# Optimization experiments

Hardware: AMD Instinct MI355X
Metric: run time of the kernel (lower is better)

Reference implementation:

```python
import jax, jax.numpy as jnp
import numpy as np
from jax import lax

EPS = 1e-06
K = 7  # kernel_size
C1 = 0.01 ** 2
C2 = 0.03 ** 2

_SOBEL_X = jnp.array([[-1.0, 0.0, 1.0], [-2.0, 0.0, 2.0], [-1.0, 0.0, 1.0]], dtype=jnp.float32).reshape(1, 1, 3, 3)
_SOBEL_Y = jnp.array([[-1.0, -2.0, -1.0], [0.0, 0.0, 0.0], [1.0, 2.0, 1.0]], dtype=jnp.float32).reshape(1, 1, 3, 3)


def _conv3x3(x, w):
    # NCHW cross-correlation with zero padding=1 (matches F.conv2d)
    return lax.conv_general_dilated(
        x, w, window_strides=(1, 1), padding=[(1, 1), (1, 1)],
        dimension_numbers=('NCHW', 'OIHW', 'NCHW'))


def _box(x):
    # avg_pool2d(k, stride=1, pad=k//2, count_include_pad=True):
    # sum over zero-padded window, divide by k*k everywhere.
    p = K // 2
    s = lax.reduce_window(x, jnp.float32(0.0), lax.add,
                          window_dimensions=(1, 1, K, K),
                          window_strides=(1, 1, 1, 1),
                          padding=[(0, 0), (0, 0), (p, p), (p, p)])
    return s / jnp.float32(K * K)


def _grad_mag(x):
    gx = _conv3x3(x, _SOBEL_X)
    gy = _conv3x3(x, _SOBEL_Y)
    return jnp.sqrt(gx * gx + gy * gy + EPS)


def setup_inputs() -> dict:
    key = jax.random.key(0)
    k1, k2 = jax.random.split(key)
    B, H, W = 64, 512, 512
    pred = jax.random.normal(k1, (B, 1, H, W), dtype=jnp.float32)
    target = jax.random.normal(k2, (B, 1, H, W), dtype=jnp.float32)
    min_target = jnp.zeros((B,), dtype=jnp.float32)
    max_target = jnp.ones((B,), dtype=jnp.float32)
    return {"pred": pred, "target": target, "min_target": min_target, "max_target": max_target}


def reference(pred, target, min_target, max_target):
    B = pred.shape[0]
    mn = min_target.reshape(B, 1, 1, 1)
    mx = max_target.reshape(B, 1, 1, 1)
    dr = jnp.maximum(mx - mn, EPS)
    p = (pred - mn) / dr
    t = (target - mn) / dr

    gp = _grad_mag(p)
    gt = _grad_mag(t)

    mu_p = _box(p)
    mu_t = _box(t)
    luminance = (2.0 * mu_p * mu_t + C1) / (mu_p * mu_p + mu_t * mu_t + C1)

    mu_gp = _box(gp)
    mu_gt = _box(gt)
    sig_p = _box(gp * gp) - mu_gp * mu_gp
    sig_t = _box(gt * gt) - mu_gt * mu_gt
    sig_x = _box(gp * gt) - mu_gp * mu_gt
    cs = (2.0 * sig_x + C2) / (sig_p + sig_t + C2)

    return 1.0 - jnp.mean(luminance * cs)
```

## Files before the change

### kernel.cpp

```cpp
#include <hip/hip_runtime.h>
#include <hip/hip_fp16.h>
#include <math.h>


constexpr int NT = 256;
constexpr float EPS_F = 1e-6f;
constexpr float C1S = 2401.0f * 0.0001f;
constexpr float C2S = 2401.0f * 0.0009f;

union U4 { uint4 u; __half2 h[4]; };
union F4U { float4 v; float a[4]; };

__device__ __forceinline__ __half2 h2swap(__half2 x) {
    unsigned u = __builtin_bit_cast(unsigned, x);
    u = (u >> 16) | (u << 16);
    return __builtin_bit_cast(__half2, u);
}

__device__ __forceinline__ float ssim_px(__half2 apt, __half2 ag, __half2 agg, __half2 agx) {
    float2 vpt = __half22float2(apt);
    float2 vg  = __half22float2(ag);
    float2 vgg = __half22float2(agg);
    float  vgx = __low2float(agx);
    float lum_n = 2.0f * vpt.x * vpt.y + C1S;
    float lum_d = vpt.x * vpt.x + vpt.y * vpt.y + C1S;
    float cs_n  = 2.0f * (49.0f * vgx - vg.x * vg.y) + C2S;
    float cs_d  = 49.0f * (vgg.x + vgg.y) - vg.x * vg.x - vg.y * vg.y + C2S;
    return lum_n * cs_n * __builtin_amdgcn_rcpf(lum_d * cs_d);
}

__global__ __launch_bounds__(NT, 4)
void gssim_strip(const float* __restrict__ pred, const float* __restrict__ target,
                 const float* __restrict__ mn_arr, const float* __restrict__ mx_arr,
                 float* __restrict__ partial) {
    constexpr int H = 512, W = 512;
    __shared__ alignas(16) __half2 spt[40][44];
    __shared__ alignas(16) __half2 sg[38][40];
    __shared__ alignas(16) __half2 hsAll[38][32][4];

    const int blk  = blockIdx.x;
    const int b    = blk >> 5;
    const int rem  = blk & 31;
    const int gy0  = (rem >> 1) * 32;
    const int tx0  = (rem & 1) * 8;
    const int tid  = threadIdx.x;

    const float mn     = mn_arr[b];
    const float inv_dr = 1.0f / fmaxf(mx_arr[b] - mn, EPS_F);
    const __half2 mn2  = __float2half2_rn(mn);
    const __half2 inv2 = __float2half2_rn(inv_dr);
    const float* pimg = pred   + (size_t)b * H * W;
    const float* timg = target + (size_t)b * H * W;

    const bool rows_ok_all = (gy0 >= 4) && (gy0 + 35 < H);

    const int gS  = tid % 10;
    const int yr  = tid / 10;
    const int yS0 = 2 * yr, yS1 = yS0 + 1;
    const int gyS0 = gy0 - 4 + yS0;
    const int gyS1 = gyS0 + 1;
    const bool rok0 = (gyS0 >= 0 && gyS0 < H);
    const bool rok1 = (gyS1 >= 0 && gyS1 < H);
    const bool hasS = (tid < 200);

    F4U Pa0, Ta0, Pa1, Ta1;

    auto stage1m = [&](int gx0n, bool rowok, int gyI, F4U& P, F4U& T) {
        int gx = gx0n - 4 + 4 * gS;
        P.v = make_float4(0.f, 0.f, 0.f, 0.f);
        T.v = make_float4(0.f, 0.f, 0.f, 0.f);
        if (rowok) {
            if (gx >= 0 && gx + 4 <= W) {
                P.v = *reinterpret_cast<const float4*>(pimg + (size_t)gyI * W + gx);
                T.v = *reinterpret_cast<const float4*>(timg + (size_t)gyI * W + gx);
            } else {
#pragma unroll
                for (int c = 0; c < 4; ++c) {
                    int x = gx + c;
                    if (x >= 0 && x < W) {
                        P.a[c] = pimg[(size_t)gyI * W + x];
                        T.a[c] = timg[(size_t)gyI * W + x];
                    }
                }
            }
        }
    };
    auto stagePair = [&](int gx0n) {
        if (rows_ok_all && gx0n >= 4 && gx0n <= 448) {
            int gx = gx0n - 4 + 4 * gS;
            Pa0.v = *reinterpret_cast<const float4*>(pimg + (size_t)gyS0 * W + gx);
            Ta0.v = *reinterpret_cast<const float4*>(timg + (size_t)gyS0 * W + gx);
            Pa1.v = *reinterpret_cast<const float4*>(pimg + (size_t)gyS1 * W + gx);
            Ta1.v = *reinterpret_cast<const float4*>(timg + (size_t)gyS1 * W + gx);
        } else {
            stage1m(gx0n, rok0, gyS0, Pa0, Ta0);
            stage1m(gx0n, rok1, gyS1, Pa1, Ta1);
        }
    };

    auto normh2 = [&](float p, float t) {
        return __hmul2(__hsub2(__floats2half2_rn(p, t), mn2), inv2);
    };
    auto writePair = [&](int gx0n) {
        U4 w0, w1;
        if (rows_ok_all && gx0n >= 4 && gx0n <= 448) {
#pragma unroll
            for (int c = 0; c < 4; ++c) {
                w0.h[c] = normh2(Pa0.a[c], Ta0.a[c]);
                w1.h[c] = normh2(Pa1.a[c], Ta1.a[c]);
            }
        } else {
            int gx = gx0n - 4 + 4 * gS;
            const __half2 zero2l = __float2half2_rn(0.0f);
#pragma unroll
            for (int c = 0; c < 4; ++c) {
                int x = gx + c;
                bool okc = (x >= 0) && (x < W);
                w0.h[c] = (rok0 && okc) ? normh2(Pa0.a[c], Ta0.a[c]) : zero2l;
                w1.h[c] = (rok1 && okc) ? normh2(Pa1.a[c], Ta1.a[c]) : zero2l;
            }
        }
        *reinterpret_cast<uint4*>(&spt[yS0][4 * gS]) = w0.u;
        *reinterpret_cast<uint4*>(&spt[yS1][4 * gS]) = w1.u;
    };

    const __half2 two2  = __float2half2_rn(2.0f);
    const __half2 eps2  = __float2half2_rn(1e-6f);
    const __half2 zero2 = __float2half2_rn(0.0f);

    if (hasS) { stagePair(tx0 * 32); writePair(tx0 * 32); }
    __syncthreads();

    float accl = 0.0f;

    for (int tt = 0; tt < 8; ++tt) {
        const int gx0 = (tx0 + tt) * 32;
        const bool interior = rows_ok_all && (gx0 >= 32) && (gx0 <= 448);

        if (tt < 7 && hasS) stagePair(gx0 + 32);

        if (tid < 190) {
            const int g  = tid % 10, kr = tid / 10;
            const int j0 = 4 * g, k0 = 2 * kr;
            __half2 a[4][6];
#pragma unroll
            for (int r = 0; r < 4; ++r) {
                U4 v; v.u = *reinterpret_cast<const uint4*>(&spt[k0 + r][j0]);
                a[r][0] = v.h[0]; a[r][1] = v.h[1]; a[r][2] = v.h[2]; a[r][3] = v.h[3];
                uint2 v2 = *reinterpret_cast<const uint2*>(&spt[k0 + r][j0 + 4]);
                a[r][4] = __builtin_bit_cast(__half2, v2.x);
                a[r][5] = __builtin_bit_cast(__half2, v2.y);
            }
            if (interior) {
#pragma unroll
                for (int rr = 0; rr < 2; ++rr) {
                    const int k = k0 + rr;
                    U4 w;
#pragma unroll
                    for (int c = 0; c < 4; ++c) {
                        __half2 gxh = __hsub2(a[rr][c + 2], a[rr][c]);
                        gxh = __hfma2(two2, __hsub2(a[rr + 1][c + 2], a[rr + 1][c]), gxh);
                        gxh = __hadd2(gxh, __hsub2(a[rr + 2][c + 2], a[rr + 2][c]));
                        __half2 gyh = __hsub2(a[rr + 2][c], a[rr][c]);
                        gyh = __hfma2(two2, __hsub2(a[rr + 2][c + 1], a[rr][c + 1]), gyh);
                        gyh = __hadd2(gyh, __hsub2(a[rr + 2][c + 2], a[rr][c + 2]));
                        w.h[c] = h2sqrt(__hfma2(gxh, gxh, __hfma2(gyh, gyh, eps2)));
                    }
                    *reinterpret_cast<uint4*>(&sg[k][j0]) = w.u;
                }
            } else {
                bool cm[4];
#pragma unroll
                for (int c = 0; c < 4; ++c) {
                    int gc = gx0 + j0 + c - 3;
                    cm[c] = (gc >= 0 && gc < W);
                }
#pragma unroll
                for (int rr = 0; rr < 2; ++rr) {
                    const int k = k0 + rr;
                    const int gr = gy0 + k - 3;
                    U4 w; w.h[0] = zero2; w.h[1] = zero2; w.h[2] = zero2; w.h[3] = zero2;
                    if (gr >= 0 && gr < H) {
#pragma unroll
                        for (int c = 0; c < 4; ++c) {
                            __half2 gxh = __hsub2(a[rr][c + 2], a[rr][c]);
                            gxh = __hfma2(two2, __hsub2(a[rr + 1][c + 2], a[rr + 1][c]), gxh);
                            gxh = __hadd2(gxh, __hsub2(a[rr + 2][c + 2], a[rr + 2][c]));
                            __half2 gyh = __hsub2(a[rr + 2][c], a[rr][c]);
                            gyh = __hfma2(two2, __hsub2(a[rr + 2][c + 1], a[rr][c + 1]), gyh);
                            gyh = __hadd2(gyh, __hsub2(a[rr + 2][c + 2], a[rr][c + 2]));
                            __half2 mag = h2sqrt(__hfma2(gxh, gxh, __hfma2(gyh, gyh, eps2)));
                            w.h[c] = cm[c] ? mag : zero2;
                        }
                    }
                    *reinterpret_cast<uint4*>(&sg[k][j0]) = w.u;
                }
            }
        }
        __syncthreads();

        auto p3unit = [&](int t) {
            const int cg = t / 38;
            const int k  = t - cg * 38;
            const int c0 = 4 * cg;
            __half2 ptv[12], sgv[12];
#pragma unroll
            for (int q = 0; q < 3; ++q) {
                U4 v; v.u = *reinterpret_cast<const uint4*>(&spt[k + 1][c0 + 4 * q]);
                ptv[4 * q] = v.h[0]; ptv[4 * q + 1] = v.h[1]; ptv[4 * q + 2] = v.h[2]; ptv[4 * q + 3] = v.h[3];
                U4 u; u.u = *reinterpret_cast<const uint4*>(&sg[k][c0 + 4 * q]);
                sgv[4 * q] = u.h[0]; sgv[4 * q + 1] = u.h[1]; sgv[4 * q + 2] = u.h[2]; sgv[4 * q + 3] = u.h[3];
            }
            __half2 gg[10], gx2[10];
#pragma unroll
            for (int q = 0; q < 10; ++q) {
                gg[q]  = __hmul2(sgv[q], sgv[q]);
                gx2[q] = __hmul2(sgv[q], h2swap(sgv[q]));
            }
            __half2 Hpt = ptv[1], Hg = sgv[0], Hgg = gg[0], Hgx = gx2[0];
#pragma unroll
            for (int q = 1; q < 7; ++q) {
                Hpt = __hadd2(Hpt, ptv[q + 1]);
                Hg  = __hadd2(Hg,  sgv[q]);
                Hgg = __hadd2(Hgg, gg[q]);
                Hgx = __hadd2(Hgx, gx2[q]);
            }
            U4 w0;
            w0.h[0] = Hpt; w0.h[1] = Hg; w0.h[2] = Hgg; w0.h[3] = Hgx;
            *reinterpret_cast<uint4*>(&hsAll[k][(c0 + k) & 31][0]) = w0.u;
#pragma unroll
            for (int m = 1; m < 4; ++m) {
                Hpt = __hadd2(__hsub2(Hpt, ptv[m]),      ptv[m + 7]);
                Hg  = __hadd2(__hsub2(Hg,  sgv[m - 1]),  sgv[m + 6]);
                Hgg = __hadd2(__hsub2(Hgg, gg[m - 1]),   gg[m + 6]);
                Hgx = __hadd2(__hsub2(Hgx, gx2[m - 1]),  gx2[m + 6]);
                U4 w;
                w.h[0] = Hpt; w.h[1] = Hg; w.h[2] = Hgg; w.h[3] = Hgx;
                *reinterpret_cast<uint4*>(&hsAll[k][(c0 + m + k) & 31][0]) = w.u;
            }
        };
        p3unit(tid);
        if (tid < 48) p3unit(tid + 256);
        __syncthreads();

        {
            const int ox = tid & 31;
            const int q  = tid >> 5;
            const int r0 = 4 * q;
            U4 win[10];
#pragma unroll
            for (int j = 0; j < 7; ++j) {
                int r = r0 + j;
                win[j].u = *reinterpret_cast<const uint4*>(&hsAll[r][(ox + r) & 31][0]);
            }
            __half2 Spt = win[0].h[0], Sg = win[0].h[1], Sgg = win[0].h[2], Sgx = win[0].h[3];
#pragma unroll
            for (int j = 1; j < 7; ++j) {
                Spt = __hadd2(Spt, win[j].h[0]);
                Sg  = __hadd2(Sg,  win[j].h[1]);
                Sgg = __hadd2(Sgg, win[j].h[2]);
                Sgx = __hadd2(Sgx, win[j].h[3]);
            }
            accl += ssim_px(Spt, Sg, Sgg, Sgx);
#pragma unroll
            for (int s = 1; s < 4; ++s) {
                int r = r0 + 6 + s;
                win[6 + s].u = *reinterpret_cast<const uint4*>(&hsAll[r][(ox + r) & 31][0]);
                Spt = __hadd2(__hsub2(Spt, win[s - 1].h[0]), win[6 + s].h[0]);
                Sg  = __hadd2(__hsub2(Sg,  win[s - 1].h[1]), win[6 + s].h[1]);
                Sgg = __hadd2(__hsub2(Sgg, win[s - 1].h[2]), win[6 + s].h[2]);
                Sgx = __hadd2(__hsub2(Sgx, win[s - 1].h[3]), win[6 + s].h[3]);
                accl += ssim_px(Spt, Sg, Sgg, Sgx);
            }
        }

        if (tt < 7 && hasS) writePair(gx0 + 32);
        __syncthreads();
    }

    float* red = reinterpret_cast<float*>(&spt[0][0]);
#pragma unroll
    for (int off = 32; off > 0; off >>= 1) accl += __shfl_down(accl, off, 64);
    if ((tid & 63) == 0) red[tid >> 6] = accl;
    __syncthreads();
    if (tid == 0) partial[blk] = red[0] + red[1] + red[2] + red[3];
}

__global__ __launch_bounds__(256)
void gssim_final(const float* __restrict__ partial, int n,
                 float* __restrict__ out, double inv_count) {
    __shared__ double sred[256];
    double acc = 0.0;
    for (int i = threadIdx.x; i < n; i += 256) acc += (double)partial[i];
    sred[threadIdx.x] = acc;
    __syncthreads();
    for (int s = 128; s > 0; s >>= 1) {
        if ((int)threadIdx.x < s) sred[threadIdx.x] += sred[threadIdx.x + s];
        __syncthreads();
    }
    if (threadIdx.x == 0) out[0] = (float)(1.0 - sred[0] * inv_count);
}

extern "C" void kernel_launch(void* const* d_in, const int* in_sizes, int n_in,
                              void* d_out, int out_size, void* d_ws, size_t ws_size,
                              hipStream_t stream) {
    const float* pred   = (const float*)d_in[0];
    const float* target = (const float*)d_in[1];
    const float* mn     = (const float*)d_in[2];
    const float* mx     = (const float*)d_in[3];
    float* out = (float*)d_out;

    const int B = in_sizes[2];
    const int H = 512, W = 512;

    float* partial = (float*)d_ws;

    const int nblocks = B * (H / 32) * 2;
    gssim_strip<<<nblocks, NT, 0, stream>>>(pred, target, mn, mx, partial);

    const double inv_count = 1.0 / ((double)B * (double)H * (double)W);
    gssim_final<<<1, 256, 0, stream>>>(partial, nblocks, out, inv_count);
}
```

Before: 71.43 us.

## Use 16-row full-width strips per block to cut LDS and raise occupancy

Each block now covers a 16-row strip across the full 512-pixel width, walking 16 column tiles, where it previously covered a 32-row strip over half the width. Shared-memory arrays shrink to match and launch bounds ask for 8 blocks per SM instead of 4. The aim is higher occupancy and a smaller LDS footprint. In exchange the vertical halo overhead per output row doubles (22 rows loaded per 16 produced), and fewer threads do useful work in each phase.

```diff
diff --git a/kernel.cpp b/kernel.cpp
--- a/kernel.cpp
+++ b/kernel.cpp
@@ -29,20 +29,18 @@
     return lum_n * cs_n * __builtin_amdgcn_rcpf(lum_d * cs_d);
 }
 
-__global__ __launch_bounds__(NT, 4)
+__global__ __launch_bounds__(NT, 8)
 void gssim_strip(const float* __restrict__ pred, const float* __restrict__ target,
                  const float* __restrict__ mn_arr, const float* __restrict__ mx_arr,
                  float* __restrict__ partial) {
     constexpr int H = 512, W = 512;
-    __shared__ alignas(16) __half2 spt[40][44];
-    __shared__ alignas(16) __half2 sg[38][40];
-    __shared__ alignas(16) __half2 hsAll[38][32][4];
+    __shared__ alignas(16) __half2 spt[24][44];
+    __shared__ alignas(16) __half2 sg[22][40];
+    __shared__ alignas(16) __half2 hsAll[22][32][4];
 
     const int blk  = blockIdx.x;
     const int b    = blk >> 5;
-    const int rem  = blk & 31;
-    const int gy0  = (rem >> 1) * 32;
-    const int tx0  = (rem & 1) * 8;
+    const int gy0  = (blk & 31) * 16;
     const int tid  = threadIdx.x;
 
     const float mn     = mn_arr[b];
@@ -52,7 +50,7 @@
     const float* pimg = pred   + (size_t)b * H * W;
     const float* timg = target + (size_t)b * H * W;
 
-    const bool rows_ok_all = (gy0 >= 4) && (gy0 + 35 < H);
+    const bool rows_ok_all = (gy0 >= 4) && (gy0 + 19 < H);
 
     const int gS  = tid % 10;
     const int yr  = tid / 10;
@@ -61,7 +59,7 @@
     const int gyS1 = gyS0 + 1;
     const bool rok0 = (gyS0 >= 0 && gyS0 < H);
     const bool rok1 = (gyS1 >= 0 && gyS1 < H);
-    const bool hasS = (tid < 200);
+    const bool hasS = (tid < 120);
 
     F4U Pa0, Ta0, Pa1, Ta1;
 
@@ -128,18 +126,18 @@
     const __half2 eps2  = __float2half2_rn(1e-6f);
     const __half2 zero2 = __float2half2_rn(0.0f);
 
-    if (hasS) { stagePair(tx0 * 32); writePair(tx0 * 32); }
+    if (hasS) { stagePair(0); writePair(0); }
     __syncthreads();
 
     float accl = 0.0f;
 
-    for (int tt = 0; tt < 8; ++tt) {
-        const int gx0 = (tx0 + tt) * 32;
+    for (int tt = 0; tt < 16; ++tt) {
+        const int gx0 = tt * 32;
         const bool interior = rows_ok_all && (gx0 >= 32) && (gx0 <= 448);
 
-        if (tt < 7 && hasS) stagePair(gx0 + 32);
-
-        if (tid < 190) {
+        if (tt < 15 && hasS) stagePair(gx0 + 32);
+
+        if (tid < 110) {
             const int g  = tid % 10, kr = tid / 10;
             const int j0 = 4 * g, k0 = 2 * kr;
             __half2 a[4][6];
@@ -199,9 +197,9 @@
         }
         __syncthreads();
 
-        auto p3unit = [&](int t) {
-            const int cg = t / 38;
-            const int k  = t - cg * 38;
+        if (tid < 176) {
+            const int cg = tid / 22;
+            const int k  = tid - cg * 22;
             const int c0 = 4 * cg;
             __half2 ptv[12], sgv[12];
 #pragma unroll
@@ -238,16 +236,13 @@
                 w.h[0] = Hpt; w.h[1] = Hg; w.h[2] = Hgg; w.h[3] = Hgx;
                 *reinterpret_cast<uint4*>(&hsAll[k][(c0 + m + k) & 31][0]) = w.u;
             }
-        };
-        p3unit(tid);
-        if (tid < 48) p3unit(tid + 256);
+        }
         __syncthreads();
 
         {
             const int ox = tid & 31;
-            const int q  = tid >> 5;
-            const int r0 = 4 * q;
-            U4 win[10];
+            const int r0 = 2 * (tid >> 5);
+            U4 win[8];
 #pragma unroll
             for (int j = 0; j < 7; ++j) {
                 int r = r0 + j;
@@ -262,19 +257,18 @@
                 Sgx = __hadd2(Sgx, win[j].h[3]);
             }
             accl += ssim_px(Spt, Sg, Sgg, Sgx);
-#pragma unroll
-            for (int s = 1; s < 4; ++s) {
-                int r = r0 + 6 + s;
-                win[6 + s].u = *reinterpret_cast<const uint4*>(&hsAll[r][(ox + r) & 31][0]);
-                Spt = __hadd2(__hsub2(Spt, win[s - 1].h[0]), win[6 + s].h[0]);
-                Sg  = __hadd2(__hsub2(Sg,  win[s - 1].h[1]), win[6 + s].h[1]);
-                Sgg = __hadd2(__hsub2(Sgg, win[s - 1].h[2]), win[6 + s].h[2]);
-                Sgx = __hadd2(__hsub2(Sgx, win[s - 1].h[3]), win[6 + s].h[3]);
+            {
+                int r = r0 + 7;
+                win[7].u = *reinterpret_cast<const uint4*>(&hsAll[r][(ox + r) & 31][0]);
+                Spt = __hadd2(__hsub2(Spt, win[0].h[0]), win[7].h[0]);
+                Sg  = __hadd2(__hsub2(Sg,  win[0].h[1]), win[7].h[1]);
+                Sgg = __hadd2(__hsub2(Sgg, win[0].h[2]), win[7].h[2]);
+                Sgx = __hadd2(__hsub2(Sgx, win[0].h[3]), win[7].h[3]);
                 accl += ssim_px(Spt, Sg, Sgg, Sgx);
             }
         }
 
-        if (tt < 7 && hasS) writePair(gx0 + 32);
+        if (tt < 15 && hasS) writePair(gx0 + 32);
         __syncthreads();
     }
 
@@ -315,7 +309,7 @@
 
     float* partial = (float*)d_ws;
 
-    const int nblocks = B * (H / 32) * 2;
+    const int nblocks = B * (H / 16);
     gssim_strip<<<nblocks, NT, 0, stream>>>(pred, target, mn, mx, partial);
 
     const double inv_count = 1.0 / ((double)B * (double)H * (double)W);
```

After: 235.7 us. 230% more time.
